# Kernel tuning notes

Measured on AMD Instinct MI355X. Metric: run time of the kernel, lower is better.

## Reference

```python
import jax, jax.numpy as jnp
import numpy as np

SIZE = 1024
INPUT_SIZE = 1024
CONTEXT_SIZE = 512
CMS = 6            # context_map_size -> 2**6 = 64 weight slots per neuron
BATCH = 128
LR = 0.01
OUT_CLIP = 0.01
W_CLIP = 5.0


def setup_inputs() -> dict:
    key = jax.random.key(0)
    k1, k2, k3, k4, k5, k6 = jax.random.split(key, 6)
    logits = jax.random.normal(k1, (INPUT_SIZE, BATCH), dtype=jnp.float32)
    context_inputs = jax.random.normal(k2, (CONTEXT_SIZE, BATCH), dtype=jnp.float32)
    targets = jax.random.uniform(k3, (BATCH,), dtype=jnp.float32)
    # learned/fixed parameters (GLN params are non-trainable buffers in torch)
    projection = 0.1 * jax.random.normal(k4, (SIZE, CMS, CONTEXT_SIZE), dtype=jnp.float32)
    projection = projection / jnp.linalg.norm(projection, axis=2, keepdims=True)
    projection_bias = 0.1 * jax.random.normal(k5, (SIZE, CMS, 1), dtype=jnp.float32)
    weights = jnp.full((SIZE, 2 ** CMS, INPUT_SIZE), 1.0 / INPUT_SIZE, dtype=jnp.float32)
    bias = jax.random.uniform(k6, (), dtype=jnp.float32, minval=OUT_CLIP, maxval=1.0 - OUT_CLIP)
    return {"logits": logits, "context_inputs": context_inputs, "targets": targets,
            "projection": projection, "projection_bias": projection_bias,
            "weights": weights, "bias": bias}


def reference(logits, context_inputs, targets, projection, projection_bias, weights, bias):
    # context hashing: (size,cms,ctx) @ (ctx,batch) -> (size,cms,batch)
    projected = jnp.einsum('smc,cb->smb', projection, context_inputs)
    bits = (projected > projection_bias).astype(jnp.int32)
    bool_conv = (2 ** jnp.arange(CMS, dtype=jnp.int32))[None, :, None]  # (1,cms,1)
    ctx_idx = jnp.sum(bits * bool_conv, axis=1)  # (size, batch) in [0, 2**cms)
    # gather per-(neuron, sample) weight rows: (size, batch, input_size)
    sel_w = jnp.take_along_axis(weights, ctx_idx[:, :, None], axis=1)
    # batched dot (torch does full matmul + diagonal; same math, done directly)
    out = jnp.einsum('sbi,ib->sb', sel_w, logits)  # (size, batch)
    out = out.at[0].set(bias)  # bias neuron overwrites row 0
    # online weight update + scatter back
    sigmoids = jnp.clip(jax.nn.sigmoid(out), OUT_CLIP, 1.0 - OUT_CLIP)
    upd = LR * (sigmoids - targets[None, :])[:, :, None] * logits.T[None, :, :]  # (size,batch,input)
    new_sel = jnp.clip(sel_w - upd, -W_CLIP, W_CLIP)
    rows = jnp.arange(SIZE)[:, None]
    new_weights = weights.at[rows, ctx_idx].set(new_sel)
    return jnp.squeeze(out), new_weights
```

## Files before the change

kernel.cpp:

```cpp
#include <hip/hip_runtime.h>

#define GLN_SIZE 1024
#define GLN_INPUT 1024
#define GLN_CTX 512
#define GLN_CMS 6
#define GLN_NCTX 64
#define GLN_BATCH 128
#define GLN_LR 0.01f
#define GLN_OUT_CLIP 0.01f
#define GLN_W_CLIP 5.0f

typedef float f32x4 __attribute__((ext_vector_type(4)));

__global__ __launch_bounds__(256) void transpose_kernel(
    const float* __restrict__ in,
    float* __restrict__ out)
{
    __shared__ float tile[32][33];
    const int bx = blockIdx.x * 32;
    const int by = blockIdx.y * 32;
    const int tx = threadIdx.x;
    const int ty = threadIdx.y;
#pragma unroll
    for (int j = 0; j < 32; j += 8) {
        int r = by + ty + j;
        int c = bx + tx;
        tile[ty + j][tx] = in[r * GLN_BATCH + c];
    }
    __syncthreads();
#pragma unroll
    for (int j = 0; j < 32; j += 8) {
        int b = bx + ty + j;
        int r = by + tx;
        out[b * GLN_INPUT + r] = tile[tx][ty + j];
    }
}

__global__ __launch_bounds__(128) void hash_kernel(
    const float* __restrict__ ctx,
    const float* __restrict__ proj,
    const float* __restrict__ pbias,
    int* __restrict__ idx)
{
    const int s = blockIdx.x;
    const int b = threadIdx.x;

    __shared__ float pl[GLN_CMS][GLN_CTX];
    const f32x4* p4 = (const f32x4*)(proj + (size_t)s * GLN_CMS * GLN_CTX);
    f32x4* pl4 = (f32x4*)&pl[0][0];
#pragma unroll
    for (int t = b; t < GLN_CMS * GLN_CTX / 4; t += 128) pl4[t] = p4[t];
    __syncthreads();

    float acc[GLN_CMS] = {0.f, 0.f, 0.f, 0.f, 0.f, 0.f};
    for (int c = 0; c < GLN_CTX; ++c) {
        float v = ctx[c * GLN_BATCH + b];
#pragma unroll
        for (int m = 0; m < GLN_CMS; ++m) acc[m] += pl[m][c] * v;
    }
    int v = 0;
#pragma unroll
    for (int m = 0; m < GLN_CMS; ++m)
        v |= (acc[m] > pbias[s * GLN_CMS + m]) ? (1 << m) : 0;
    idx[s * GLN_BATCH + b] = v;
}

__global__ __launch_bounds__(512, 4) void gln_kernel(
    const float* __restrict__ weights,
    const float* __restrict__ logitsT,
    const float* __restrict__ targets,
    const float* __restrict__ biasPtr,
    const int* __restrict__ idx,
    float* __restrict__ outv,
    float* __restrict__ outw)
{
    const int s    = blockIdx.x;
    const int tid  = threadIdx.x;
    const int lane = tid & 63;
    const int wv   = tid >> 6;

    __shared__ int cnt[GLN_NCTX];
    __shared__ int winner[GLN_NCTX];
    __shared__ unsigned char lists[GLN_NCTX][GLN_BATCH];

    if (tid < GLN_NCTX) { cnt[tid] = 0; winner[tid] = -1; }
    __syncthreads();
    if (tid < GLN_BATCH) {
        int c = idx[s * GLN_BATCH + tid];
        int slot = atomicAdd(&cnt[c], 1);
        lists[c][slot] = (unsigned char)tid;
        atomicMax(&winner[c], tid);
    }
    __syncthreads();

    const float bias = biasPtr[0];
    const float* wrow_base = weights + (size_t)s * GLN_NCTX * GLN_INPUT;
    float*       orow_base = outw    + (size_t)s * GLN_NCTX * GLN_INPUT;

    f32x4 w4[4], w4n[4];
    {
        const f32x4* wr = (const f32x4*)(wrow_base + (wv * 8) * GLN_INPUT);
#pragma unroll
        for (int k = 0; k < 4; ++k)
            w4[k] = __builtin_nontemporal_load(wr + lane + k * 64);
    }

#pragma unroll
    for (int ci = 0; ci < 8; ++ci) {
        const int c = wv * 8 + ci;

        if (ci < 7) {
            const f32x4* wrn = (const f32x4*)(wrow_base + (c + 1) * GLN_INPUT);
#pragma unroll
            for (int k = 0; k < 4; ++k)
                w4n[k] = __builtin_nontemporal_load(wrn + lane + k * 64);
        }

        const int n    = cnt[c];
        const int bwin = winner[c];
        float dwin = 0.0f;

        for (int u = 0; u < n; ++u) {
            const int b = lists[c][u];
            float outval;
            if (s != 0) {
                const f32x4* lg = (const f32x4*)(logitsT + b * GLN_INPUT);
                float p = 0.f;
#pragma unroll
                for (int k = 0; k < 4; ++k) {
                    f32x4 g = lg[lane + k * 64];
                    p += w4[k][0] * g[0] + w4[k][1] * g[1] +
                         w4[k][2] * g[2] + w4[k][3] * g[3];
                }
#pragma unroll
                for (int off = 1; off < 64; off <<= 1)
                    p += __shfl_xor(p, off, 64);
                outval = p;
            } else {
                outval = bias;
            }
            float sg = 1.0f / (1.0f + expf(-outval));
            sg = fminf(fmaxf(sg, GLN_OUT_CLIP), 1.0f - GLN_OUT_CLIP);
            float d = GLN_LR * (sg - targets[b]);
            if (lane == 0) outv[s * GLN_BATCH + b] = outval;
            if (b == bwin) dwin = d;
        }

        f32x4* orow = (f32x4*)(orow_base + c * GLN_INPUT);
        if (bwin >= 0) {
            const f32x4* lg = (const f32x4*)(logitsT + bwin * GLN_INPUT);
#pragma unroll
            for (int k = 0; k < 4; ++k) {
                f32x4 g = lg[lane + k * 64];
                f32x4 r;
                r[0] = fminf(fmaxf(w4[k][0] - dwin * g[0], -GLN_W_CLIP), GLN_W_CLIP);
                r[1] = fminf(fmaxf(w4[k][1] - dwin * g[1], -GLN_W_CLIP), GLN_W_CLIP);
                r[2] = fminf(fmaxf(w4[k][2] - dwin * g[2], -GLN_W_CLIP), GLN_W_CLIP);
                r[3] = fminf(fmaxf(w4[k][3] - dwin * g[3], -GLN_W_CLIP), GLN_W_CLIP);
                __builtin_nontemporal_store(r, orow + lane + k * 64);
            }
        } else {
#pragma unroll
            for (int k = 0; k < 4; ++k)
                __builtin_nontemporal_store(w4[k], orow + lane + k * 64);
        }

#pragma unroll
        for (int k = 0; k < 4; ++k) w4[k] = w4n[k];
    }
}

extern "C" void kernel_launch(void* const* d_in, const int* in_sizes, int n_in,
                              void* d_out, int out_size, void* d_ws, size_t ws_size,
                              hipStream_t stream) {
    const float* logits  = (const float*)d_in[0];
    const float* ctx     = (const float*)d_in[1];
    const float* targets = (const float*)d_in[2];
    const float* proj    = (const float*)d_in[3];
    const float* pbias   = (const float*)d_in[4];
    const float* weights = (const float*)d_in[5];
    const float* bias    = (const float*)d_in[6];

    float* outv = (float*)d_out;
    float* outw = outv + GLN_SIZE * GLN_BATCH;

    float* logitsT = (float*)d_ws;
    int*   idx     = (int*)(logitsT + GLN_BATCH * GLN_INPUT);

    transpose_kernel<<<dim3(GLN_BATCH / 32, GLN_INPUT / 32), dim3(32, 8), 0, stream>>>(
        logits, logitsT);
    hash_kernel<<<GLN_SIZE, 128, 0, stream>>>(ctx, proj, pbias, idx);
    gln_kernel<<<GLN_SIZE, 512, 0, stream>>>(weights, logitsT, targets, bias,
                                             idx, outv, outw);
}
```

Baseline: 511.1 us.

## Split GLN neurons across two blocks, pair dot products, transpose context for hashing

The main kernel now launches two 256-thread blocks per neuron, each handling 32 of the 64 context rows, to raise block count and occupancy. The per-sample dot product loop handles two samples at a time so their loads and shuffles interleave. Weight loads lose the nontemporal hint. The context input is transposed so the hash kernel reads projection rows directly with vector loads instead of staging them in shared memory. This adds one more launch, and each half-block redoes the bucket histogram.

Result: slower. 531.7 us (+4.0%).

```diff
diff --git a/kernel.cpp b/kernel.cpp
--- a/kernel.cpp
+++ b/kernel.cpp
@@ -13,8 +13,7 @@
 typedef float f32x4 __attribute__((ext_vector_type(4)));
 
 __global__ __launch_bounds__(256) void transpose_kernel(
-    const float* __restrict__ in,
-    float* __restrict__ out)
+    const float* __restrict__ in, float* __restrict__ out, int R, int C)
 {
     __shared__ float tile[32][33];
     const int bx = blockIdx.x * 32;
@@ -22,22 +21,16 @@
     const int tx = threadIdx.x;
     const int ty = threadIdx.y;
 #pragma unroll
-    for (int j = 0; j < 32; j += 8) {
-        int r = by + ty + j;
-        int c = bx + tx;
-        tile[ty + j][tx] = in[r * GLN_BATCH + c];
-    }
+    for (int j = 0; j < 32; j += 8)
+        tile[ty + j][tx] = in[(by + ty + j) * C + (bx + tx)];
     __syncthreads();
 #pragma unroll
-    for (int j = 0; j < 32; j += 8) {
-        int b = bx + ty + j;
-        int r = by + tx;
-        out[b * GLN_INPUT + r] = tile[tx][ty + j];
-    }
+    for (int j = 0; j < 32; j += 8)
+        out[(bx + ty + j) * R + (by + tx)] = tile[tx][ty + j];
 }
 
 __global__ __launch_bounds__(128) void hash_kernel(
-    const float* __restrict__ ctx,
+    const float* __restrict__ ctxT,
     const float* __restrict__ proj,
     const float* __restrict__ pbias,
     int* __restrict__ idx)
@@ -45,18 +38,20 @@
     const int s = blockIdx.x;
     const int b = threadIdx.x;
 
-    __shared__ float pl[GLN_CMS][GLN_CTX];
-    const f32x4* p4 = (const f32x4*)(proj + (size_t)s * GLN_CMS * GLN_CTX);
-    f32x4* pl4 = (f32x4*)&pl[0][0];
-#pragma unroll
-    for (int t = b; t < GLN_CMS * GLN_CTX / 4; t += 128) pl4[t] = p4[t];
-    __syncthreads();
+    const f32x4* ct = (const f32x4*)(ctxT + (size_t)b * GLN_CTX);
+    const f32x4* pr = (const f32x4*)(proj + (size_t)s * GLN_CMS * GLN_CTX);
 
     float acc[GLN_CMS] = {0.f, 0.f, 0.f, 0.f, 0.f, 0.f};
-    for (int c = 0; c < GLN_CTX; ++c) {
-        float v = ctx[c * GLN_BATCH + b];
-#pragma unroll
-        for (int m = 0; m < GLN_CMS; ++m) acc[m] += pl[m][c] * v;
+    for (int c4 = 0; c4 < GLN_CTX / 4; ++c4) {
+        f32x4 v = ct[c4];
+#pragma unroll
+        for (int m = 0; m < GLN_CMS; ++m) {
+            f32x4 p = pr[m * (GLN_CTX / 4) + c4];
+            acc[m] += p[0] * v[0];
+            acc[m] += p[1] * v[1];
+            acc[m] += p[2] * v[2];
+            acc[m] += p[3] * v[3];
+        }
     }
     int v = 0;
 #pragma unroll
@@ -65,7 +60,53 @@
     idx[s * GLN_BATCH + b] = v;
 }
 
-__global__ __launch_bounds__(512, 4) void gln_kernel(
+__device__ __forceinline__ float dot_row(const f32x4* __restrict__ lg,
+                                         const f32x4 w4[4], int lane)
+{
+    float p = 0.f;
+#pragma unroll
+    for (int k = 0; k < 4; ++k) {
+        f32x4 g = lg[lane + k * 64];
+        p += w4[k][0] * g[0] + w4[k][1] * g[1] +
+             w4[k][2] * g[2] + w4[k][3] * g[3];
+    }
+#pragma unroll
+    for (int off = 1; off < 64; off <<= 1)
+        p += __shfl_xor(p, off, 64);
+    return p;
+}
+
+__device__ __forceinline__ void dot_row2(const f32x4* __restrict__ la,
+                                         const f32x4* __restrict__ lb,
+                                         const f32x4 w4[4], int lane,
+                                         float& pa, float& pb)
+{
+    float a = 0.f, b = 0.f;
+#pragma unroll
+    for (int k = 0; k < 4; ++k) {
+        f32x4 ga = la[lane + k * 64];
+        f32x4 gb = lb[lane + k * 64];
+        a += w4[k][0] * ga[0] + w4[k][1] * ga[1] +
+             w4[k][2] * ga[2] + w4[k][3] * ga[3];
+        b += w4[k][0] * gb[0] + w4[k][1] * gb[1] +
+             w4[k][2] * gb[2] + w4[k][3] * gb[3];
+    }
+#pragma unroll
+    for (int off = 1; off < 64; off <<= 1) {
+        a += __shfl_xor(a, off, 64);
+        b += __shfl_xor(b, off, 64);
+    }
+    pa = a; pb = b;
+}
+
+__device__ __forceinline__ float delta_of(float outval, float tgt)
+{
+    float sg = 1.0f / (1.0f + expf(-outval));
+    sg = fminf(fmaxf(sg, GLN_OUT_CLIP), 1.0f - GLN_OUT_CLIP);
+    return GLN_LR * (sg - tgt);
+}
+
+__global__ __launch_bounds__(256) void gln_kernel(
     const float* __restrict__ weights,
     const float* __restrict__ logitsT,
     const float* __restrict__ targets,
@@ -74,7 +115,8 @@
     float* __restrict__ outv,
     float* __restrict__ outw)
 {
-    const int s    = blockIdx.x;
+    const int s    = blockIdx.x >> 1;
+    const int half = blockIdx.x & 1;
     const int tid  = threadIdx.x;
     const int lane = tid & 63;
     const int wv   = tid >> 6;
@@ -96,52 +138,58 @@
     const float bias = biasPtr[0];
     const float* wrow_base = weights + (size_t)s * GLN_NCTX * GLN_INPUT;
     float*       orow_base = outw    + (size_t)s * GLN_NCTX * GLN_INPUT;
+    const int rowbase = half * 32 + wv * 8;
 
     f32x4 w4[4], w4n[4];
     {
-        const f32x4* wr = (const f32x4*)(wrow_base + (wv * 8) * GLN_INPUT);
-#pragma unroll
-        for (int k = 0; k < 4; ++k)
-            w4[k] = __builtin_nontemporal_load(wr + lane + k * 64);
+        const f32x4* wr = (const f32x4*)(wrow_base + rowbase * GLN_INPUT);
+#pragma unroll
+        for (int k = 0; k < 4; ++k) w4[k] = wr[lane + k * 64];
     }
 
 #pragma unroll
     for (int ci = 0; ci < 8; ++ci) {
-        const int c = wv * 8 + ci;
+        const int c = rowbase + ci;
 
         if (ci < 7) {
             const f32x4* wrn = (const f32x4*)(wrow_base + (c + 1) * GLN_INPUT);
 #pragma unroll
-            for (int k = 0; k < 4; ++k)
-                w4n[k] = __builtin_nontemporal_load(wrn + lane + k * 64);
+            for (int k = 0; k < 4; ++k) w4n[k] = wrn[lane + k * 64];
         }
 
         const int n    = cnt[c];
         const int bwin = winner[c];
         float dwin = 0.0f;
 
-        for (int u = 0; u < n; ++u) {
+        int u = 0;
+        for (; u + 1 < n; u += 2) {
+            const int ba = lists[c][u];
+            const int bb = lists[c][u + 1];
+            float oa, ob;
+            if (s != 0) {
+                dot_row2((const f32x4*)(logitsT + ba * GLN_INPUT),
+                         (const f32x4*)(logitsT + bb * GLN_INPUT),
+                         w4, lane, oa, ob);
+            } else {
+                oa = bias; ob = bias;
+            }
+            float da = delta_of(oa, targets[ba]);
+            float db = delta_of(ob, targets[bb]);
+            if (lane == 0) {
+                outv[s * GLN_BATCH + ba] = oa;
+                outv[s * GLN_BATCH + bb] = ob;
+            }
+            if (ba == bwin) dwin = da;
+            if (bb == bwin) dwin = db;
+        }
+        if (u < n) {
             const int b = lists[c][u];
             float outval;
-            if (s != 0) {
-                const f32x4* lg = (const f32x4*)(logitsT + b * GLN_INPUT);
-                float p = 0.f;
-#pragma unroll
-                for (int k = 0; k < 4; ++k) {
-                    f32x4 g = lg[lane + k * 64];
-                    p += w4[k][0] * g[0] + w4[k][1] * g[1] +
-                         w4[k][2] * g[2] + w4[k][3] * g[3];
-                }
-#pragma unroll
-                for (int off = 1; off < 64; off <<= 1)
-                    p += __shfl_xor(p, off, 64);
-                outval = p;
-            } else {
+            if (s != 0)
+                outval = dot_row((const f32x4*)(logitsT + b * GLN_INPUT), w4, lane);
+            else
                 outval = bias;
-            }
-            float sg = 1.0f / (1.0f + expf(-outval));
-            sg = fminf(fmaxf(sg, GLN_OUT_CLIP), 1.0f - GLN_OUT_CLIP);
-            float d = GLN_LR * (sg - targets[b]);
+            float d = delta_of(outval, targets[b]);
             if (lane == 0) outv[s * GLN_BATCH + b] = outval;
             if (b == bwin) dwin = d;
         }
@@ -185,11 +233,14 @@
     float* outw = outv + GLN_SIZE * GLN_BATCH;
 
     float* logitsT = (float*)d_ws;
-    int*   idx     = (int*)(logitsT + GLN_BATCH * GLN_INPUT);
+    float* ctxT    = logitsT + GLN_BATCH * GLN_INPUT;
+    int*   idx     = (int*)(ctxT + GLN_BATCH * GLN_CTX);
 
     transpose_kernel<<<dim3(GLN_BATCH / 32, GLN_INPUT / 32), dim3(32, 8), 0, stream>>>(
-        logits, logitsT);
-    hash_kernel<<<GLN_SIZE, 128, 0, stream>>>(ctx, proj, pbias, idx);
-    gln_kernel<<<GLN_SIZE, 512, 0, stream>>>(weights, logitsT, targets, bias,
-                                             idx, outv, outw);
-}
+        logits, logitsT, GLN_INPUT, GLN_BATCH);
+    transpose_kernel<<<dim3(GLN_BATCH / 32, GLN_CTX / 32), dim3(32, 8), 0, stream>>>(
+        ctx, ctxT, GLN_CTX, GLN_BATCH);
+    hash_kernel<<<GLN_SIZE, 128, 0, stream>>>(ctxT, proj, pbias, idx);
+    gln_kernel<<<GLN_SIZE * 2, 256, 0, stream>>>(weights, logitsT, targets, bias,
+                                                 idx, outv, outw);
+}
```
